# Performance work log

Measured on AMD Instinct MI355X. Metric: run time of the kernel, lower is better.

## Reference

```python
import jax, jax.numpy as jnp
import numpy as np

T, B, NS, NC = 100, 4096, 12, 4
N = NS + NC  # tau dim


def setup_inputs() -> dict:
    key = jax.random.key(0)
    k1, k2, k3, k4, k5 = jax.random.split(key, 5)
    # Symmetric PD quadratic cost C = L L^T / N + I  -> well conditioned
    L = jax.random.normal(k1, (T, B, N, N), dtype=jnp.float32) * 0.1
    C = jnp.einsum('tbij,tbkj->tbik', L, L) + jnp.eye(N, dtype=jnp.float32)
    c = jax.random.normal(k2, (T, B, N), dtype=jnp.float32)
    # Linear dynamics x' = F [x;u] + f, state block near identity for stability
    F = jax.random.normal(k3, (T - 1, B, NS, N), dtype=jnp.float32) * 0.02
    A0 = jnp.concatenate([0.99 * jnp.eye(NS, dtype=jnp.float32),
                          jnp.zeros((NS, NC), jnp.float32)], axis=-1)
    F = F + A0  # broadcast over (T-1, B)
    f = jax.random.normal(k4, (T - 1, B, NS), dtype=jnp.float32) * 0.01
    x_init = jax.random.normal(k5, (B, NS), dtype=jnp.float32)
    return {"x_init": x_init, "C": C, "c": c, "F": F, "f": f}


def _lqr_solve(x_init, C, c, F, f):
    ns = x_init.shape[-1]
    # Pad dynamics to length T (terminal step has no dynamics; V starts at 0
    # so the padded zero F/f contribute nothing).
    Fp = jnp.concatenate([F, jnp.zeros_like(F[:1])], axis=0)  # [T,B,ns,n]
    fp = jnp.concatenate([f, jnp.zeros_like(f[:1])], axis=0)  # [T,B,ns]

    def bwd_step(carry, inp):
        V, v = carry                      # [B,ns,ns], [B,ns]
        Ct, ct, Ft, ft = inp
        # Q = C + F^T V F ; q = c + F^T (V f + v)
        Q = Ct + jnp.einsum('bsi,bst,btj->bij', Ft, V, Ft)
        Vf = jnp.einsum('bst,bt->bs', V, ft) + v
        q = ct + jnp.einsum('bsi,bs->bi', Ft, Vf)
        Qxx, Qxu = Q[:, :ns, :ns], Q[:, :ns, ns:]
        Qux, Quu = Q[:, ns:, :ns], Q[:, ns:, ns:]
        qx, qu = q[:, :ns], q[:, ns:]
        # Joint solve for K = -Quu^{-1} Qux, k = -Quu^{-1} qu
        Kk = -jnp.linalg.solve(Quu, jnp.concatenate([Qux, qu[..., None]], axis=-1))
        K, k = Kk[..., :ns], Kk[..., ns]
        Vn = Qxx + jnp.einsum('bij,bjk->bik', Qxu, K)
        Vn = 0.5 * (Vn + jnp.swapaxes(Vn, -1, -2))
        vn = qx + jnp.einsum('bij,bj->bi', Qxu, k)
        return (Vn, vn), (K, k)

    V0 = jnp.zeros((x_init.shape[0], ns, ns), C.dtype)
    v0 = jnp.zeros((x_init.shape[0], ns), C.dtype)
    _, (Kr, kr) = jax.lax.scan(bwd_step, (V0, v0),
                               (C[::-1], c[::-1], Fp[::-1], fp[::-1]))
    K, k = Kr[::-1], kr[::-1]  # [T,B,nc,ns], [T,B,nc]

    def fwd_step(x, inp):
        Ct, ct, Ft, ft, Kt, kt = inp
        u = jnp.einsum('bij,bj->bi', Kt, x) + kt
        tau = jnp.concatenate([x, u], axis=-1)
        cost = 0.5 * jnp.einsum('bi,bij,bj->b', tau, Ct, tau) \
               + jnp.einsum('bi,bi->b', ct, tau)
        xn = jnp.einsum('bij,bj->bi', Ft, tau) + ft
        return xn, (x, u, cost)

    _, (xs, us, costs) = jax.lax.scan(fwd_step, x_init, (C, c, Fp, fp, K, k))
    return xs, us, jnp.sum(costs, axis=0)


def reference(x_init, C, c, F, f):
    # MPC with QuadCost + LinDx and no box constraints: the iLQR loop
    # converges in one exact LQR solve (Riccati backward + forward rollout).
    x, u, objs = _lqr_solve(x_init, C, c, F, f)
    return x, u, objs
```

## Files before the change

kernel.cpp:

```cpp
#include <hip/hip_runtime.h>
#include <hip/hip_fp16.h>

#define TT 100
#define BB 4096
#define GS 520


#define FENCE() asm volatile("s_waitcnt lgkmcnt(0)" ::: "memory")

__device__ __forceinline__ float pairsum32(float x){
  float a=x, b=x;
  asm("v_permlane32_swap_b32 %0, %1" : "+v"(a), "+v"(b));
  return a+b;
}

template<int KMODE>
__device__ __forceinline__ void storeK(void* wsv, size_t of, int l, float X0,float X1,float X2,float X3){
  if (KMODE==0){
    float* wsb=(float*)wsv + of*52;
    if (l<12)       ((float4*)wsb)[l]  = make_float4(X0,X1,X2,X3);
    else if (l==12) ((float4*)wsb)[12] = make_float4(X0,X1,X2,X3);
  } else {
    __half* wsb=(__half*)wsv + of*52;
    if (l<12){
      wsb[l*4+0]=__float2half(X0); wsb[l*4+1]=__float2half(X1);
      wsb[l*4+2]=__float2half(X2); wsb[l*4+3]=__float2half(X3);
    } else if (l==12){
      wsb[48]=__float2half(X0); wsb[49]=__float2half(X1);
      wsb[50]=__float2half(X2); wsb[51]=__float2half(X3);
    }
  }
}
template<int KMODE>
__device__ __forceinline__ float4 loadKcol(const void* wsv, size_t of, int l){
  if (KMODE==0) return ((const float4*)((const float*)wsv + of*52))[l];
  const __half* p=(const __half*)wsv + of*52 + l*4;
  return make_float4(__half2float(p[0]),__half2float(p[1]),__half2float(p[2]),__half2float(p[3]));
}
template<int KMODE>
__device__ __forceinline__ float loadkk(const void* wsv, size_t of, int r){
  if (KMODE==0) return ((const float*)wsv)[of*52+48+r];
  return __half2float(((const __half*)wsv)[of*52+48+r]);
}

template<int KMODE>
__global__ __launch_bounds__(256)
void lqr_fused(const float* __restrict__ xinit,
               const float* __restrict__ Cg,
               const float* __restrict__ cg,
               const float* __restrict__ Fg,
               const float* __restrict__ fg,
               float* __restrict__ out,
               void* __restrict__ wsv)
{
  __shared__ float smem[GS*8];
  const int tid    = threadIdx.x;
  const int lane   = tid & 63;
  const int l      = lane & 15;
  const int h      = lane >> 5;
  const int w      = (lane >> 4) & 1;
  const int gi     = (tid >> 6)*2 + w;
  const int b      = blockIdx.x*8 + gi;
  const int base16 = lane & 16;

  float* __restrict__ V   = smem + gi*GS;
  float* __restrict__ Fl  = V + 144;
  float* __restrict__ Qxu = V + 384;
  float* __restrict__ Quu = V + 432;
  float* __restrict__ vv  = V + 448;
  float* __restrict__ tb  = V + 460;

  float4 sCa,sCb; float sc_;
  float4 sFa=make_float4(0,0,0,0),sFb=sFa; float sf_=0.f;
  {
    const size_t of = ((size_t)(TT-1)*BB + b);
    const float4* pc = (const float4*)(Cg + of*256 + l*16);
    sCa=pc[2*h]; sCb=pc[2*h+1];
    sc_ = cg[of*16 + l];
  }

  for (int tt=TT-1; tt>=0; --tt){
    const bool hasF = (tt < TT-1);
    float4 Ca=sCa,Cb=sCb; float rc=sc_;
    float4 Fa=sFa,Fb=sFb; float rf=sf_;

    if (hasF && l<12){
      float4* q=(float4*)(Fl + l*20);
      q[2*h]=Fa; q[2*h+1]=Fb;
      if (h==0) tb[l]=rf;
    }
    FENCE();

    if (tt>0){
      const size_t of = ((size_t)(tt-1)*BB + b);
      const float4* pc=(const float4*)(Cg + of*256 + l*16);
      sCa=pc[2*h]; sCb=pc[2*h+1];
      sc_=cg[of*16+l];
      if (l<12){
        const float4* pf=(const float4*)(Fg + of*192 + l*16);
        sFa=pf[2*h]; sFb=pf[2*h+1];
        if (h==0) sf_=fg[of*12+l];
      }
    }

    const float R0=Ca.x,R1=Ca.y,R2=Ca.z,R3=Ca.w,R4=Cb.x,R5=Cb.y,R6=Cb.z,R7=Cb.w;
    float Qp[16];
    Qp[0]=h?0.f:R0; Qp[1]=h?0.f:R1; Qp[2]=h?0.f:R2; Qp[3]=h?0.f:R3;
    Qp[4]=h?0.f:R4; Qp[5]=h?0.f:R5; Qp[6]=h?0.f:R6; Qp[7]=h?0.f:R7;
    Qp[8]=h?R0:0.f; Qp[9]=h?R1:0.f; Qp[10]=h?R2:0.f; Qp[11]=h?R3:0.f;
    Qp[12]=h?R4:0.f; Qp[13]=h?R5:0.f; Qp[14]=h?R6:0.f; Qp[15]=h?R7:0.f;
    float qvp = h? 0.f : rc;

    if (hasF){
      float FtL[6], FtH[6];
      #pragma unroll
      for (int k2=0;k2<6;k2++){ FtL[k2]=Fl[k2*20+l]; FtH[k2]=Fl[(6+k2)*20+l]; }
      const int s0=6*h;
      float Wl[6];
      #pragma unroll
      for (int k2=0;k2<6;k2++){
        const float4* vr=(const float4*)(V+(s0+k2)*12);
        float4 v0=vr[0],v1=vr[1],v2=vr[2];
        Wl[k2]= v0.x*FtL[0]+v0.y*FtL[1]+v0.z*FtL[2]+v0.w*FtL[3]
              + v1.x*FtL[4]+v1.y*FtL[5]+v1.z*FtH[0]+v1.w*FtH[1]
              + v2.x*FtH[2]+v2.y*FtH[3]+v2.z*FtH[4]+v2.w*FtH[5];
      }
      #pragma unroll
      for (int k2=0;k2<6;k2++){
        const float4* fr=(const float4*)(Fl + (s0+k2)*20);
        float4 f0=fr[0],f1=fr[1],f2=fr[2],f3=fr[3];
        float w2=Wl[k2];
        Qp[0]+=f0.x*w2;  Qp[1]+=f0.y*w2;  Qp[2]+=f0.z*w2;  Qp[3]+=f0.w*w2;
        Qp[4]+=f1.x*w2;  Qp[5]+=f1.y*w2;  Qp[6]+=f1.z*w2;  Qp[7]+=f1.w*w2;
        Qp[8]+=f2.x*w2;  Qp[9]+=f2.y*w2;  Qp[10]+=f2.z*w2; Qp[11]+=f2.w*w2;
        Qp[12]+=f3.x*w2; Qp[13]+=f3.y*w2; Qp[14]+=f3.z*w2; Qp[15]+=f3.w*w2;
      }
      #pragma unroll
      for (int k2=0;k2<6;k2++){
        qvp += Wl[k2]*tb[s0+k2];
        const float ftk = h? FtH[k2] : FtL[k2];
        qvp += ftk * vv[s0+k2];
      }
    }

    float Qc[16];
    #pragma unroll
    for (int i=0;i<16;i++) Qc[i] = pairsum32(Qp[i]);
    float qv = pairsum32(qvp);

    if (h==0 && l>=12){
      const int cc=l-12;
      ((float4*)Quu)[cc] = make_float4(Qc[12],Qc[13],Qc[14],Qc[15]);
      float4* qx=(float4*)(Qxu + cc*12);
      qx[0]=make_float4(Qc[0],Qc[1],Qc[2],Qc[3]);
      qx[1]=make_float4(Qc[4],Qc[5],Qc[6],Qc[7]);
      qx[2]=make_float4(Qc[8],Qc[9],Qc[10],Qc[11]);
    }
    FENCE();

    float qu0=__shfl(qv,base16+12,64),qu1=__shfl(qv,base16+13,64),
          qu2=__shfl(qv,base16+14,64),qu3=__shfl(qv,base16+15,64);
    float b0,b1,b2,b3;
    if (l<12){b0=-Qc[12];b1=-Qc[13];b2=-Qc[14];b3=-Qc[15];}
    else     {b0=-qu0;b1=-qu1;b2=-qu2;b3=-qu3;}

    const float4 quu0=((const float4*)Quu)[0], quu1=((const float4*)Quu)[1],
                 quu2=((const float4*)Quu)[2], quu3=((const float4*)Quu)[3];
    float a00=quu0.x,a10=quu0.y,a20=quu0.z,a30=quu0.w;
    float a01=quu1.x,a11=quu1.y,a21=quu1.z,a31=quu1.w;
    float a02=quu2.x,a12=quu2.y,a22=quu2.z,a32=quu2.w;
    float a03=quu3.x,a13=quu3.y,a23=quu3.z,a33=quu3.w;

    float i0=1.0f/a00;
    float m10=a10*i0,m20=a20*i0,m30=a30*i0;
    a11-=m10*a01;a12-=m10*a02;a13-=m10*a03;b1-=m10*b0;
    a21-=m20*a01;a22-=m20*a02;a23-=m20*a03;b2-=m20*b0;
    a31-=m30*a01;a32-=m30*a02;a33-=m30*a03;b3-=m30*b0;
    float i1=1.0f/a11;
    float m21=a21*i1,m31=a31*i1;
    a22-=m21*a12;a23-=m21*a13;b2-=m21*b1;
    a32-=m31*a12;a33-=m31*a13;b3-=m31*b1;
    float i2=1.0f/a22;
    float m32=a32*i2;
    a33-=m32*a23;b3-=m32*b2;
    float X3=b3/a33;
    float X2=(b2-a23*X3)*i2;
    float X1=(b1-a12*X2-a13*X3)*i1;
    float X0=(b0-a01*X1-a02*X2-a03*X3)*i0;

    if (h==0) storeK<KMODE>(wsv, (size_t)tt*BB+b, l, X0,X1,X2,X3);

    const float k0=__shfl(X0,base16+12,64),k1=__shfl(X1,base16+12,64),
                k2=__shfl(X2,base16+12,64),k3=__shfl(X3,base16+12,64);

    if (l<12){
      const int i0i=6*h;
      float Vn[6];
      #pragma unroll
      for (int k2=0;k2<6;k2++) Vn[k2] = h? Qc[6+k2] : Qc[k2];
      #pragma unroll
      for (int r=0;r<4;r++){
        const float Xr=(r==0)?X0:(r==1)?X1:(r==2)?X2:X3;
        const float2* qx2=(const float2*)(Qxu + r*12 + i0i);
        float2 x0=qx2[0],x1=qx2[1],x2=qx2[2];
        Vn[0]+=x0.x*Xr; Vn[1]+=x0.y*Xr; Vn[2]+=x1.x*Xr;
        Vn[3]+=x1.y*Xr; Vn[4]+=x2.x*Xr; Vn[5]+=x2.y*Xr;
      }
      #pragma unroll
      for (int k2=0;k2<6;k2++) V[(i0i+k2)*12+l]=Vn[k2];
      if (h==0){
        vv[l] = qv + Qc[12]*k0 + Qc[13]*k1 + Qc[14]*k2 + Qc[15]*k3;
      }
    }
  }

  asm volatile("s_waitcnt vmcnt(0)" ::: "memory");

  float xj = (h==0 && l<12)? xinit[(size_t)b*12+l] : 0.f;
  double costacc=0.0;

  float4 sF0=make_float4(0,0,0,0),sF1=sF0,sF2=sF0,sF3=sF0;
  float4 sK=make_float4(0,0,0,0); float sk_=0.f;
  {
    const float4* pc=(const float4*)(Cg + (size_t)b*256 + l*16);
    sCa=pc[2*h]; sCb=pc[2*h+1];
    sc_=cg[(size_t)b*16+l];
    if (h==0 && l<12){
      const float4* pf=(const float4*)(Fg + (size_t)b*192 + l*16);
      sF0=pf[0];sF1=pf[1];sF2=pf[2];sF3=pf[3];
      sf_=fg[(size_t)b*12+l];
      sK=loadKcol<KMODE>(wsv,(size_t)b,l);
    }
    if (h==0 && l>=12) sk_=loadkk<KMODE>(wsv,(size_t)b,l-12);
  }

  for (int t=0;t<TT;t++){
    float4 Ca=sCa,Cb=sCb; float rc=sc_;
    float4 F0=sF0,F1=sF1,F2=sF2,F3=sF3; float rf=sf_;
    float4 K4=sK; float kl=sk_;

    if (t+1<TT){
      const size_t of=((size_t)(t+1)*BB + b);
      const float4* pc=(const float4*)(Cg + of*256 + l*16);
      sCa=pc[2*h]; sCb=pc[2*h+1];
      sc_=cg[of*16+l];
      if (h==0 && l<12){
        sK=loadKcol<KMODE>(wsv,of,l);
        if (t+1<TT-1){
          const float4* pf=(const float4*)(Fg + of*192 + l*16);
          sF0=pf[0];sF1=pf[1];sF2=pf[2];sF3=pf[3];
          sf_=fg[of*12+l];
        }
      }
      if (h==0 && l>=12) sk_=loadkk<KMODE>(wsv,of,l-12);
    }

    float pr0=0.f,pr1=0.f,pr2=0.f,pr3=0.f;
    if (h==0 && l<12){ pr0=K4.x*xj; pr1=K4.y*xj; pr2=K4.z*xj; pr3=K4.w*xj; }
    #pragma unroll
    for (int m=1;m<16;m<<=1){
      pr0+=__shfl_xor(pr0,m,64); pr1+=__shfl_xor(pr1,m,64);
      pr2+=__shfl_xor(pr2,m,64); pr3+=__shfl_xor(pr3,m,64);
    }
    float* tbuf = tb + (t&1)*16;
    float tauj=0.f;
    if (h==0){
      if (l<12) tauj=xj;
      else {
        const float ur=(l==12)?pr0:(l==13)?pr1:(l==14)?pr2:pr3;
        tauj=ur+kl;
      }
      tbuf[l]=tauj;
    }
    FENCE();

    const float4* tp=(const float4*)tbuf;
    const float4 ta=tp[2*h], tb4=tp[2*h+1];
    const float taul = tbuf[l];

    float dot_p = Ca.x*ta.x + Ca.y*ta.y + Ca.z*ta.z + Ca.w*ta.w
                + Cb.x*tb4.x + Cb.y*tb4.y + Cb.z*tb4.z + Cb.w*tb4.w;
    costacc += (double)( taul*0.5f*dot_p + (h==0 ? taul*rc : 0.f) );

    if (h==0){
      if (l<12) out[(size_t)t*BB*12 + (size_t)b*12 + l] = xj;
      else      out[(size_t)TT*BB*12 + (size_t)t*BB*4 + (size_t)b*4 + (l-12)] = tauj;
    }

    if (t<TT-1 && h==0 && l<12){
      const float4 t0=tp[0],t1=tp[1],t2=tp[2],t3=tp[3];
      xj = rf
         + F0.x*t0.x+F0.y*t0.y+F0.z*t0.z+F0.w*t0.w
         + F1.x*t1.x+F1.y*t1.y+F1.z*t1.z+F1.w*t1.w
         + F2.x*t2.x+F2.y*t2.y+F2.z*t2.z+F2.w*t2.w
         + F3.x*t3.x+F3.y*t3.y+F3.z*t3.z+F3.w*t3.w;
    }
  }

  costacc+=__shfl_xor(costacc,1,64); costacc+=__shfl_xor(costacc,2,64);
  costacc+=__shfl_xor(costacc,4,64); costacc+=__shfl_xor(costacc,8,64);
  costacc+=__shfl_xor(costacc,32,64);
  if (h==0 && l==0) out[(size_t)TT*BB*16 + b]=(float)costacc;
}

extern "C" void kernel_launch(void* const* d_in, const int* in_sizes, int n_in,
                              void* d_out, int out_size, void* d_ws, size_t ws_size,
                              hipStream_t stream){
  (void)in_sizes; (void)n_in; (void)out_size;
  const float* xinit=(const float*)d_in[0];
  const float* C    =(const float*)d_in[1];
  const float* c    =(const float*)d_in[2];
  const float* F    =(const float*)d_in[3];
  const float* f    =(const float*)d_in[4];
  const size_t need_f32 = (size_t)TT*BB*52*sizeof(float);
  if (ws_size >= need_f32){
    lqr_fused<0><<<dim3(BB/8), dim3(256), 0, stream>>>(xinit,C,c,F,f,(float*)d_out,d_ws);
  } else {
    lqr_fused<1><<<dim3(BB/8), dim3(256), 0, stream>>>(xinit,C,c,F,f,(float*)d_out,d_ws);
  }
}
```

Baseline: 441.7 us.

## Replace cross-lane shuffles with DPP reductions and redundant per-lane k solve

Swaps the 16-lane ds_swizzle/shfl_xor reduction in the forward rollout for DPP row_ror adds. Each lane now recomputes the k vector by forward/back substitution instead of broadcasting it from lane 12 by shuffle. It also vectorises LDS reads and writes for qv and V, changes V's store layout to row-major per lane, and replaces permlane32_swap with a shfl_xor in pairsum32. Together these cut LDS/cross-lane traffic on the serial per-step critical path, at the cost of some redundant ALU. The V store layout change must match its readers, and the GS shrink alters the shared-memory footprint.

```diff
diff --git a/kernel.cpp b/kernel.cpp
--- a/kernel.cpp
+++ b/kernel.cpp
@@ -3,15 +3,25 @@
 
 #define TT 100
 #define BB 4096
-#define GS 520
-
+#define GS 516
 
 #define FENCE() asm volatile("s_waitcnt lgkmcnt(0)" ::: "memory")
 
 __device__ __forceinline__ float pairsum32(float x){
-  float a=x, b=x;
-  asm("v_permlane32_swap_b32 %0, %1" : "+v"(a), "+v"(b));
-  return a+b;
+  return x + __shfl_xor(x, 32, 64);
+}
+
+template<int CTRL>
+__device__ __forceinline__ float ror_add(float x){
+  int r = __builtin_amdgcn_update_dpp(0, __float_as_int(x), CTRL, 0xF, 0xF, true);
+  return x + __int_as_float(r);
+}
+__device__ __forceinline__ float reduce16_dpp(float x){
+  x = ror_add<0x128>(x);
+  x = ror_add<0x124>(x);
+  x = ror_add<0x122>(x);
+  x = ror_add<0x121>(x);
+  return x;
 }
 
 template<int KMODE>
@@ -103,12 +113,12 @@
       }
     }
 
-    const float R0=Ca.x,R1=Ca.y,R2=Ca.z,R3=Ca.w,R4=Cb.x,R5=Cb.y,R6=Cb.z,R7=Cb.w;
+    const float R0=Ca.x,R1=Ca.y,R2=Ca.z,R3=Ca.w,R4=Cb.x,R5=Cb.y,R6=Cb.z,R7v=Cb.w;
     float Qp[16];
     Qp[0]=h?0.f:R0; Qp[1]=h?0.f:R1; Qp[2]=h?0.f:R2; Qp[3]=h?0.f:R3;
-    Qp[4]=h?0.f:R4; Qp[5]=h?0.f:R5; Qp[6]=h?0.f:R6; Qp[7]=h?0.f:R7;
+    Qp[4]=h?0.f:R4; Qp[5]=h?0.f:R5; Qp[6]=h?0.f:R6; Qp[7]=h?0.f:R7v;
     Qp[8]=h?R0:0.f; Qp[9]=h?R1:0.f; Qp[10]=h?R2:0.f; Qp[11]=h?R3:0.f;
-    Qp[12]=h?R4:0.f; Qp[13]=h?R5:0.f; Qp[14]=h?R6:0.f; Qp[15]=h?R7:0.f;
+    Qp[12]=h?R4:0.f; Qp[13]=h?R5:0.f; Qp[14]=h?R6:0.f; Qp[15]=h?R7v:0.f;
     float qvp = h? 0.f : rc;
 
     if (hasF){
@@ -135,12 +145,15 @@
         Qp[8]+=f2.x*w2;  Qp[9]+=f2.y*w2;  Qp[10]+=f2.z*w2; Qp[11]+=f2.w*w2;
         Qp[12]+=f3.x*w2; Qp[13]+=f3.y*w2; Qp[14]+=f3.z*w2; Qp[15]+=f3.w*w2;
       }
-      #pragma unroll
-      for (int k2=0;k2<6;k2++){
-        qvp += Wl[k2]*tb[s0+k2];
-        const float ftk = h? FtH[k2] : FtL[k2];
-        qvp += ftk * vv[s0+k2];
-      }
+      const float2* tbp=(const float2*)(tb + s0);
+      const float2* vvp=(const float2*)(vv + s0);
+      const float2 t0=tbp[0],t1=tbp[1],t2=tbp[2];
+      const float2 u0=vvp[0],u1=vvp[1],u2=vvp[2];
+      qvp += Wl[0]*t0.x + Wl[1]*t0.y + Wl[2]*t1.x
+           + Wl[3]*t1.y + Wl[4]*t2.x + Wl[5]*t2.y;
+      const float g0=h?FtH[0]:FtL[0], g1=h?FtH[1]:FtL[1], g2=h?FtH[2]:FtL[2],
+                  g3=h?FtH[3]:FtL[3], g4=h?FtH[4]:FtL[4], g5=h?FtH[5]:FtL[5];
+      qvp += g0*u0.x + g1*u0.y + g2*u1.x + g3*u1.y + g4*u2.x + g5*u2.y;
     }
 
     float Qc[16];
@@ -188,10 +201,16 @@
     float X1=(b1-a12*X2-a13*X3)*i1;
     float X0=(b0-a01*X1-a02*X2-a03*X3)*i0;
 
+    float c0=-qu0,c1=-qu1,c2=-qu2,c3=-qu3;
+    c1-=m10*c0; c2-=m20*c0; c3-=m30*c0;
+    c2-=m21*c1; c3-=m31*c1;
+    c3-=m32*c2;
+    const float k3=c3/a33;
+    const float k2v=(c2-a23*k3)*i2;
+    const float k1=(c1-a12*k2v-a13*k3)*i1;
+    const float k0=(c0-a01*k1-a02*k2v-a03*k3)*i0;
+
     if (h==0) storeK<KMODE>(wsv, (size_t)tt*BB+b, l, X0,X1,X2,X3);
-
-    const float k0=__shfl(X0,base16+12,64),k1=__shfl(X1,base16+12,64),
-                k2=__shfl(X2,base16+12,64),k3=__shfl(X3,base16+12,64);
 
     if (l<12){
       const int i0i=6*h;
@@ -206,10 +225,12 @@
         Vn[0]+=x0.x*Xr; Vn[1]+=x0.y*Xr; Vn[2]+=x1.x*Xr;
         Vn[3]+=x1.y*Xr; Vn[4]+=x2.x*Xr; Vn[5]+=x2.y*Xr;
       }
-      #pragma unroll
-      for (int k2=0;k2<6;k2++) V[(i0i+k2)*12+l]=Vn[k2];
+      float2* vwr=(float2*)(V + l*12 + i0i);
+      vwr[0]=make_float2(Vn[0],Vn[1]);
+      vwr[1]=make_float2(Vn[2],Vn[3]);
+      vwr[2]=make_float2(Vn[4],Vn[5]);
       if (h==0){
-        vv[l] = qv + Qc[12]*k0 + Qc[13]*k1 + Qc[14]*k2 + Qc[15]*k3;
+        vv[l] = qv + Qc[12]*k0 + Qc[13]*k1 + Qc[14]*k2v + Qc[15]*k3;
       }
     }
   }
@@ -257,11 +278,9 @@
 
     float pr0=0.f,pr1=0.f,pr2=0.f,pr3=0.f;
     if (h==0 && l<12){ pr0=K4.x*xj; pr1=K4.y*xj; pr2=K4.z*xj; pr3=K4.w*xj; }
-    #pragma unroll
-    for (int m=1;m<16;m<<=1){
-      pr0+=__shfl_xor(pr0,m,64); pr1+=__shfl_xor(pr1,m,64);
-      pr2+=__shfl_xor(pr2,m,64); pr3+=__shfl_xor(pr3,m,64);
-    }
+    pr0=reduce16_dpp(pr0); pr1=reduce16_dpp(pr1);
+    pr2=reduce16_dpp(pr2); pr3=reduce16_dpp(pr3);
+
     float* tbuf = tb + (t&1)*16;
     float tauj=0.f;
     if (h==0){
@@ -274,9 +293,10 @@
     }
     FENCE();
 
+    const float taul = tbuf[l];
+
     const float4* tp=(const float4*)tbuf;
     const float4 ta=tp[2*h], tb4=tp[2*h+1];
-    const float taul = tbuf[l];
 
     float dot_p = Ca.x*ta.x + Ca.y*ta.y + Ca.z*ta.z + Ca.w*ta.w
                 + Cb.x*tb4.x + Cb.y*tb4.y + Cb.z*tb4.z + Cb.w*tb4.w;
```

New measurement: 445.2 us. About the same (+0.8%).
